# Optimization experiments

Hardware: AMD Instinct MI355X
Metric: run time of the kernel (lower is better)

The kernel has to match this reference:

```python
import jax, jax.numpy as jnp
import numpy as np

TOP_K = 10
RANKING_WEIGHT = 0.3
UP_WEIGHT = 1.0
DOWN_WEIGHT = 0.5
NEG = 1e9  # finite stand-in for -inf so softmax/grads stay NaN-free


def setup_inputs() -> dict:
    key = jax.random.key(0)
    k1, k2, k3, k4 = jax.random.split(key, 4)
    B, N = 1024, 5000
    up_logits = jax.random.normal(k1, (B, N), jnp.float32)
    down_logits = jax.random.normal(k2, (B, N), jnp.float32)
    y_true = jax.random.normal(k3, (B, N), jnp.float32) * 0.05  # daily returns
    masks = jax.random.randint(k4, (B, N), 0, 2).astype(jnp.int32)
    return {"up_logits": up_logits, "down_logits": down_logits,
            "y_true": y_true, "masks": masks}


def _bce_with_logits(x, z):
    # softplus(x) - x*z  ==  -[z*log(sig(x)) + (1-z)*log(1-sig(x))]
    return jax.nn.softplus(x) - x * z


def reference(up_logits, down_logits, y_true, masks):
    maskb = masks > 0                                   # [B, N]
    maskf = maskb.astype(up_logits.dtype)
    num_valid = maskf.sum(-1)                           # [B]
    nv_safe = jnp.maximum(num_valid, 1.0)
    k = jnp.minimum(TOP_K, num_valid.astype(jnp.int32))  # [B] min(top_k, num)

    # Descending rank of y_true among valid entries (invalid pushed to bottom).
    y_desc = jnp.where(maskb, y_true, -NEG)
    rank_desc = jnp.argsort(jnp.argsort(-y_desc, axis=-1), axis=-1)  # [B, N]
    up_labels = (rank_desc < k[:, None]).astype(up_logits.dtype)

    # Ascending rank (biggest losers) for down path.
    y_asc = jnp.where(maskb, y_true, NEG)
    rank_asc = jnp.argsort(jnp.argsort(y_asc, axis=-1), axis=-1)
    down_labels = (rank_asc < k[:, None]).astype(down_logits.dtype)

    # Mean BCE over valid entries per row.
    up_loss = jnp.sum(_bce_with_logits(up_logits, up_labels) * maskf, -1) / nv_safe
    down_loss = jnp.sum(_bce_with_logits(down_logits, down_labels) * maskf, -1) / nv_safe

    # Listwise KL: softmax over valid entries; kl_div(log p, q, 'batchmean')
    # with 1D input of size num divides the sum by num.
    logp = jax.nn.log_softmax(jnp.where(maskb, up_logits, -NEG), axis=-1)
    logq = jax.nn.log_softmax(jnp.where(maskb, y_true, -NEG), axis=-1)
    q = jnp.exp(logq)
    kl = jnp.sum(jnp.where(maskb, q * (logq - logp), 0.0), -1) / nv_safe

    batch_loss = UP_WEIGHT * up_loss + DOWN_WEIGHT * down_loss + RANKING_WEIGHT * kl
    batch_loss = jnp.where(num_valid > 0, batch_loss, 0.0)  # skip empty rows
    return jnp.sum(batch_loss) / up_logits.shape[0]
```

## Files before the change

### kernel.cpp

```cpp
#include <hip/hip_runtime.h>
#include <math.h>

#define NCOLS 5000
#define NF4   1250
#define BLOCK 512
#define NWAVES (BLOCK / 64)
#define NITER 3
#define TOPKK 10
#define CAP 256

__device__ __forceinline__ unsigned mono_f32(float f) {
  unsigned u = __float_as_uint(f);
  return (u & 0x80000000u) ? ~u : (u | 0x80000000u);
}

__device__ __forceinline__ float wave_sum_f(float v) {
#pragma unroll
  for (int o = 1; o < 64; o <<= 1) v += __shfl_xor(v, o);
  return v;
}
__device__ __forceinline__ int wave_sum_i(int v) {
#pragma unroll
  for (int o = 1; o < 64; o <<= 1) v += __shfl_xor(v, o);
  return v;
}
__device__ __forceinline__ unsigned wave_max_u(unsigned v) {
#pragma unroll
  for (int o = 1; o < 64; o <<= 1) {
    unsigned w = __shfl_xor(v, o);
    v = w > v ? w : v;
  }
  return v;
}

extern "C" __global__ __launch_bounds__(BLOCK, 4)
void row_loss_kernel(const float* __restrict__ up, const float* __restrict__ down,
                     const float* __restrict__ yt, const int* __restrict__ masks,
                     float* __restrict__ out, float inv_nrows) {
  __shared__ float red_f[6][NWAVES];
  __shared__ int red_i[NWAVES];
  __shared__ unsigned t1w_t[NWAVES];
  __shared__ unsigned t1w_b[NWAVES];
  __shared__ unsigned keys_t[CAP];
  __shared__ float    vals_t[CAP];
  __shared__ unsigned keys_b[CAP];
  __shared__ float    vals_b[CAP];
  __shared__ int ct, cb;
  __shared__ float s_res[2];

  const int tid = threadIdx.x;
  const int lane = tid & 63;
  const int wv = tid >> 6;
  const long long b4 = (long long)blockIdx.x * NF4;

  const float4* up4 = (const float4*)up + b4;
  const float4* dn4 = (const float4*)down + b4;
  const float4* yt4 = (const float4*)yt + b4;
  const int4*   mk4 = (const int4*)masks + b4;

  if (tid == 0) { ct = 0; cb = 0; }

  float4 y4[NITER], u4[NITER], d4[NITER];
  int4 m4[NITER];
#pragma unroll
  for (int j = 0; j < NITER; ++j) {
    const int f = j * BLOCK + tid;
    if (f < NF4) {
      y4[j] = yt4[f]; u4[j] = up4[f]; d4[j] = dn4[f]; m4[j] = mk4[f];
    } else {
      y4[j] = make_float4(0.f, 0.f, 0.f, 0.f);
      u4[j] = y4[j]; d4[j] = y4[j];
      m4[j] = make_int4(0, 0, 0, 0);
    }
  }

  unsigned km[NITER][4];
  float uu[NITER][4], dd[NITER][4];
  int nv_l = 0;
  float sq = 0.f, sp = 0.f, seyy = 0.f, seyu = 0.f, aspu = 0.f, aspd = 0.f;
  unsigned tmax = 0u, tbmax = 0u;
#pragma unroll
  for (int j = 0; j < NITER; ++j) {
    const float* yp = (const float*)&y4[j];
    const float* upp = (const float*)&u4[j];
    const float* dp = (const float*)&d4[j];
    const int* mp = (const int*)&m4[j];
#pragma unroll
    for (int c = 0; c < 4; ++c) {
      const bool valid = mp[c] > 0;
      const float y = yp[c], u = upp[c], d = dp[c];
      uu[j][c] = u;
      dd[j][c] = d;
      const unsigned kd = valid ? mono_f32(y) : 0u;
      km[j][c] = kd;
      const unsigned kb = valid ? ~kd : 0u;
      tmax = kd > tmax ? kd : tmax;
      tbmax = kb > tbmax ? kb : tbmax;
      if (valid) {
        nv_l++;
        const float ey = __expf(y);
        sq += ey;
        seyy += ey * y;
        seyu += ey * u;
        sp += __expf(u);
        aspu += fmaxf(u, 0.f) + __logf(1.f + __expf(-fabsf(u)));
        aspd += fmaxf(d, 0.f) + __logf(1.f + __expf(-fabsf(d)));
      }
    }
  }

  nv_l = wave_sum_i(nv_l);
  sq = wave_sum_f(sq);
  sp = wave_sum_f(sp);
  seyy = wave_sum_f(seyy);
  seyu = wave_sum_f(seyu);
  aspu = wave_sum_f(aspu);
  aspd = wave_sum_f(aspd);
  if (lane == 0) {
    red_i[wv] = nv_l;
    red_f[0][wv] = sq;  red_f[1][wv] = sp;
    red_f[2][wv] = seyy; red_f[3][wv] = seyu;
    red_f[4][wv] = aspu; red_f[5][wv] = aspd;
  }

  {
    unsigned v = tmax, t1 = 0u;
#pragma unroll 1
    for (int r = 0; r < TOPKK; ++r) {
      unsigned m = wave_max_u(v);
      if (v == m) v = 0u;
      t1 = m;
    }
    if (lane == 0) t1w_t[wv] = t1;
  }
  {
    unsigned v = tbmax, t1 = 0u;
#pragma unroll 1
    for (int r = 0; r < TOPKK; ++r) {
      unsigned m = wave_max_u(v);
      if (v == m) v = 0u;
      t1 = m;
    }
    if (lane == 0) t1w_b[wv] = t1;
  }
  __syncthreads();

  int nv = 0;
#pragma unroll
  for (int w = 0; w < NWAVES; ++w) nv += red_i[w];
  const int k = nv < TOPKK ? nv : TOPKK;

  unsigned t1 = 0u, t1b = 0u;
#pragma unroll
  for (int w = 0; w < NWAVES; ++w) {
    t1 = t1w_t[w] > t1 ? t1w_t[w] : t1;
    t1b = t1w_b[w] > t1b ? t1w_b[w] : t1b;
  }

#pragma unroll
  for (int j = 0; j < NITER; ++j) {
#pragma unroll
    for (int c = 0; c < 4; ++c) {
      const unsigned kd = km[j][c];
      if (kd != 0u) {
        if (kd >= t1) {
          int i = atomicAdd(&ct, 1);
          if (i < CAP) { keys_t[i] = kd; vals_t[i] = uu[j][c]; }
        }
        const unsigned kb = ~kd;
        if (kb >= t1b) {
          int i = atomicAdd(&cb, 1);
          if (i < CAP) { keys_b[i] = kb; vals_b[i] = dd[j][c]; }
        }
      }
    }
  }
  __syncthreads();

  if (wv == 0) {
    const int n = ct < CAP ? ct : CAP;
    unsigned kk[4]; float vvv[4];
#pragma unroll
    for (int i = 0; i < 4; ++i) {
      const int idx = i * 64 + lane;
      kk[i] = (idx < n) ? keys_t[idx] : 0u;
      vvv[i] = (idx < n) ? vals_t[idx] : 0.f;
    }
    unsigned w0 = kk[0], w1 = kk[1], w2 = kk[2], w3 = kk[3];
    unsigned thr = 0xFFFFFFFFu;
#pragma unroll 1
    for (int r = 0; r < k; ++r) {
      unsigned lm = w0 > w1 ? w0 : w1;
      unsigned lm2 = w2 > w3 ? w2 : w3;
      lm = lm > lm2 ? lm : lm2;
      unsigned m = wave_max_u(lm);
      if (w0 == m) w0 = 0u;
      else if (w1 == m) w1 = 0u;
      else if (w2 == m) w2 = 0u;
      else if (w3 == m) w3 = 0u;
      thr = m;
    }
    float su = 0.f;
#pragma unroll
    for (int i = 0; i < 4; ++i)
      if (kk[i] >= thr && kk[i] != 0u) su += vvv[i];
    su = wave_sum_f(su);
    if (lane == 0) s_res[0] = su;
  } else if (wv == 1) {
    const int n = cb < CAP ? cb : CAP;
    unsigned kk[4]; float vvv[4];
#pragma unroll
    for (int i = 0; i < 4; ++i) {
      const int idx = i * 64 + lane;
      kk[i] = (idx < n) ? keys_b[idx] : 0u;
      vvv[i] = (idx < n) ? vals_b[idx] : 0.f;
    }
    unsigned w0 = kk[0], w1 = kk[1], w2 = kk[2], w3 = kk[3];
    unsigned thr = 0xFFFFFFFFu;
#pragma unroll 1
    for (int r = 0; r < k; ++r) {
      unsigned lm = w0 > w1 ? w0 : w1;
      unsigned lm2 = w2 > w3 ? w2 : w3;
      lm = lm > lm2 ? lm : lm2;
      unsigned m = wave_max_u(lm);
      if (w0 == m) w0 = 0u;
      else if (w1 == m) w1 = 0u;
      else if (w2 == m) w2 = 0u;
      else if (w3 == m) w3 = 0u;
      thr = m;
    }
    float sd = 0.f;
#pragma unroll
    for (int i = 0; i < 4; ++i)
      if (kk[i] >= thr && kk[i] != 0u) sd += vvv[i];
    sd = wave_sum_f(sd);
    if (lane == 0) s_res[1] = sd;
  }
  __syncthreads();

  if (tid == 0 && nv > 0) {
    float SQ = 0.f, SP = 0.f, SYY = 0.f, SYU = 0.f, ASU = 0.f, ASD = 0.f;
#pragma unroll
    for (int w = 0; w < NWAVES; ++w) {
      SQ += red_f[0][w]; SP += red_f[1][w];
      SYY += red_f[2][w]; SYU += red_f[3][w];
      ASU += red_f[4][w]; ASD += red_f[5][w];
    }
    const float SU = s_res[0];
    const float SD = s_res[1];
    const float kl = (SYY - SYU) / SQ - __logf(SQ) + __logf(SP);
    const float up_loss = ASU - SU;
    const float dn_loss = ASD - SD;
    const float loss = (up_loss + 0.5f * dn_loss + 0.3f * kl) / (float)nv;
    atomicAdd(out, loss * inv_nrows);
  }
}

extern "C" void kernel_launch(void* const* d_in, const int* in_sizes, int n_in,
                              void* d_out, int out_size, void* d_ws, size_t ws_size,
                              hipStream_t stream) {
  const float* up_logits   = (const float*)d_in[0];
  const float* down_logits = (const float*)d_in[1];
  const float* y_true      = (const float*)d_in[2];
  const int*   masks       = (const int*)d_in[3];

  const int nrows = in_sizes[0] / NCOLS;

  hipMemsetAsync(d_out, 0, sizeof(float) * (size_t)out_size, stream);
  row_loss_kernel<<<nrows, BLOCK, 0, stream>>>(up_logits, down_logits, y_true,
                                               masks, (float*)d_out,
                                               1.0f / (float)nrows);
}
```

Baseline: 130.4 us.

## Halve block size, store candidate columns, and re-read selected logits from global

Shrinks the block to 256 threads with five float4 iterations per thread, and halves the candidate buffer capacity. Candidates now store column indices instead of logit values, so the up/down values no longer need to stay in registers until selection and are re-read from global memory (likely L2-resident) for the few selected entries. Out-of-range loads are clamped instead of branched. This trades register pressure and branch overhead for a small gather at the end, with more top-k candidates per wave in the tournament and a smaller candidate capacity.

```diff
diff --git a/kernel.cpp b/kernel.cpp
--- a/kernel.cpp
+++ b/kernel.cpp
@@ -3,11 +3,11 @@
 
 #define NCOLS 5000
 #define NF4   1250
-#define BLOCK 512
+#define BLOCK 256
 #define NWAVES (BLOCK / 64)
-#define NITER 3
+#define NITER 5
 #define TOPKK 10
-#define CAP 256
+#define CAP 128
 
 __device__ __forceinline__ unsigned mono_f32(float f) {
   unsigned u = __float_as_uint(f);
@@ -42,16 +42,18 @@
   __shared__ unsigned t1w_t[NWAVES];
   __shared__ unsigned t1w_b[NWAVES];
   __shared__ unsigned keys_t[CAP];
-  __shared__ float    vals_t[CAP];
+  __shared__ int      col_t[CAP];
   __shared__ unsigned keys_b[CAP];
-  __shared__ float    vals_b[CAP];
+  __shared__ int      col_b[CAP];
   __shared__ int ct, cb;
   __shared__ float s_res[2];
 
   const int tid = threadIdx.x;
   const int lane = tid & 63;
   const int wv = tid >> 6;
-  const long long b4 = (long long)blockIdx.x * NF4;
+  const int row = blockIdx.x;
+  const long long b4 = (long long)row * NF4;
+  const long long base = (long long)row * NCOLS;
 
   const float4* up4 = (const float4*)up + b4;
   const float4* dn4 = (const float4*)down + b4;
@@ -65,35 +67,31 @@
 #pragma unroll
   for (int j = 0; j < NITER; ++j) {
     const int f = j * BLOCK + tid;
-    if (f < NF4) {
-      y4[j] = yt4[f]; u4[j] = up4[f]; d4[j] = dn4[f]; m4[j] = mk4[f];
-    } else {
-      y4[j] = make_float4(0.f, 0.f, 0.f, 0.f);
-      u4[j] = y4[j]; d4[j] = y4[j];
-      m4[j] = make_int4(0, 0, 0, 0);
-    }
+    const int fc = f < NF4 ? f : NF4 - 1;
+    y4[j] = yt4[fc];
+    u4[j] = up4[fc];
+    d4[j] = dn4[fc];
+    m4[j] = mk4[fc];
   }
 
   unsigned km[NITER][4];
-  float uu[NITER][4], dd[NITER][4];
   int nv_l = 0;
   float sq = 0.f, sp = 0.f, seyy = 0.f, seyu = 0.f, aspu = 0.f, aspd = 0.f;
   unsigned tmax = 0u, tbmax = 0u;
 #pragma unroll
   for (int j = 0; j < NITER; ++j) {
+    const bool inb = (j * BLOCK + tid) < NF4;
     const float* yp = (const float*)&y4[j];
     const float* upp = (const float*)&u4[j];
     const float* dp = (const float*)&d4[j];
     const int* mp = (const int*)&m4[j];
 #pragma unroll
     for (int c = 0; c < 4; ++c) {
-      const bool valid = mp[c] > 0;
+      const bool valid = inb && (mp[c] > 0);
       const float y = yp[c], u = upp[c], d = dp[c];
-      uu[j][c] = u;
-      dd[j][c] = d;
       const unsigned kd = valid ? mono_f32(y) : 0u;
+      const unsigned kb = valid ? ~kd : 0u;
       km[j][c] = kd;
-      const unsigned kb = valid ? ~kd : 0u;
       tmax = kd > tmax ? kd : tmax;
       tbmax = kb > tbmax ? kb : tbmax;
       if (valid) {
@@ -163,14 +161,15 @@
     for (int c = 0; c < 4; ++c) {
       const unsigned kd = km[j][c];
       if (kd != 0u) {
+        const int col = ((j * BLOCK + tid) << 2) + c;
         if (kd >= t1) {
           int i = atomicAdd(&ct, 1);
-          if (i < CAP) { keys_t[i] = kd; vals_t[i] = uu[j][c]; }
+          if (i < CAP) { keys_t[i] = kd; col_t[i] = col; }
         }
         const unsigned kb = ~kd;
         if (kb >= t1b) {
           int i = atomicAdd(&cb, 1);
-          if (i < CAP) { keys_b[i] = kb; vals_b[i] = dd[j][c]; }
+          if (i < CAP) { keys_b[i] = kb; col_b[i] = col; }
         }
       }
     }
@@ -179,60 +178,38 @@
 
   if (wv == 0) {
     const int n = ct < CAP ? ct : CAP;
-    unsigned kk[4]; float vvv[4];
-#pragma unroll
-    for (int i = 0; i < 4; ++i) {
-      const int idx = i * 64 + lane;
-      kk[i] = (idx < n) ? keys_t[idx] : 0u;
-      vvv[i] = (idx < n) ? vals_t[idx] : 0.f;
-    }
-    unsigned w0 = kk[0], w1 = kk[1], w2 = kk[2], w3 = kk[3];
+    unsigned k0 = (lane < n) ? keys_t[lane] : 0u;
+    unsigned k1 = (64 + lane < n) ? keys_t[64 + lane] : 0u;
+    unsigned w0 = k0, w1 = k1;
     unsigned thr = 0xFFFFFFFFu;
 #pragma unroll 1
     for (int r = 0; r < k; ++r) {
-      unsigned lm = w0 > w1 ? w0 : w1;
-      unsigned lm2 = w2 > w3 ? w2 : w3;
-      lm = lm > lm2 ? lm : lm2;
-      unsigned m = wave_max_u(lm);
+      unsigned m = wave_max_u(w0 > w1 ? w0 : w1);
       if (w0 == m) w0 = 0u;
       else if (w1 == m) w1 = 0u;
-      else if (w2 == m) w2 = 0u;
-      else if (w3 == m) w3 = 0u;
       thr = m;
     }
     float su = 0.f;
-#pragma unroll
-    for (int i = 0; i < 4; ++i)
-      if (kk[i] >= thr && kk[i] != 0u) su += vvv[i];
+    if (k0 >= thr && k0 != 0u) su += up[base + col_t[lane]];
+    if (k1 >= thr && k1 != 0u) su += up[base + col_t[64 + lane]];
     su = wave_sum_f(su);
     if (lane == 0) s_res[0] = su;
   } else if (wv == 1) {
     const int n = cb < CAP ? cb : CAP;
-    unsigned kk[4]; float vvv[4];
-#pragma unroll
-    for (int i = 0; i < 4; ++i) {
-      const int idx = i * 64 + lane;
-      kk[i] = (idx < n) ? keys_b[idx] : 0u;
-      vvv[i] = (idx < n) ? vals_b[idx] : 0.f;
-    }
-    unsigned w0 = kk[0], w1 = kk[1], w2 = kk[2], w3 = kk[3];
+    unsigned k0 = (lane < n) ? keys_b[lane] : 0u;
+    unsigned k1 = (64 + lane < n) ? keys_b[64 + lane] : 0u;
+    unsigned w0 = k0, w1 = k1;
     unsigned thr = 0xFFFFFFFFu;
 #pragma unroll 1
     for (int r = 0; r < k; ++r) {
-      unsigned lm = w0 > w1 ? w0 : w1;
-      unsigned lm2 = w2 > w3 ? w2 : w3;
-      lm = lm > lm2 ? lm : lm2;
-      unsigned m = wave_max_u(lm);
+      unsigned m = wave_max_u(w0 > w1 ? w0 : w1);
       if (w0 == m) w0 = 0u;
       else if (w1 == m) w1 = 0u;
-      else if (w2 == m) w2 = 0u;
-      else if (w3 == m) w3 = 0u;
       thr = m;
     }
     float sd = 0.f;
-#pragma unroll
-    for (int i = 0; i < 4; ++i)
-      if (kk[i] >= thr && kk[i] != 0u) sd += vvv[i];
+    if (k0 >= thr && k0 != 0u) sd += down[base + col_b[lane]];
+    if (k1 >= thr && k1 != 0u) sd += down[base + col_b[64 + lane]];
     sd = wave_sum_f(sd);
     if (lane == 0) s_res[1] = sd;
   }
```

New measurement: 124.2 us. -4.8%, faster.
